# Kernel tuning notes

Hardware: AMD Instinct MI355X
Metric: run time of the kernel (lower is better)

The kernel has to match this reference:

```python
import jax, jax.numpy as jnp
import numpy as np

N_NODES = 50000
N_EDGES = 600000
K = 4
BN_EPS = 1e-5


def setup_inputs() -> dict:
    key = jax.random.key(0)
    ks = jax.random.split(key, 8)
    x = jax.random.normal(ks[0], (N_NODES, 128), dtype=jnp.float32)
    edge_index = jax.random.randint(ks[1], (2, N_EDGES), 0, N_NODES, dtype=jnp.int64)
    edge_weight = jax.random.uniform(ks[2], (N_EDGES,), dtype=jnp.float32)
    conv_w = jax.random.normal(ks[3], (10, K, 128, 128), dtype=jnp.float32)
    conv_b = jnp.zeros((10, 128), dtype=jnp.float32)
    bn_gamma = jnp.ones((10, 128), dtype=jnp.float32)
    bn_beta = jnp.zeros((10, 128), dtype=jnp.float32)
    lin_w = jax.random.normal(ks[4], (128, 16), dtype=jnp.float32)
    lin_b = jnp.zeros((16,), dtype=jnp.float32)
    return {"x": x, "edge_index": edge_index, "edge_weight": edge_weight,
            "conv_w": conv_w, "conv_b": conv_b, "bn_gamma": bn_gamma,
            "bn_beta": bn_beta, "lin_w": lin_w, "lin_b": lin_b}


def _cheb_norm(edge_index, edge_weight, n_nodes):
    # PyG ChebConv with lambda_max=2, sym normalization:
    # L_hat = 2L/lambda_max - I = -D^{-1/2} A D^{-1/2}, zero diagonal.
    row, col = edge_index[0], edge_index[1]
    w = jnp.where(row == col, 0.0, edge_weight)  # remove_self_loops
    deg = jax.ops.segment_sum(w, row, num_segments=n_nodes)
    dis = jnp.where(deg > 0, jax.lax.rsqrt(jnp.where(deg > 0, deg, 1.0)), 0.0)
    norm = -dis[row] * w * dis[col]
    return norm


def _propagate(h, norm, src, dst, n_nodes):
    # (L_hat h)[i] = sum over edges (src->dst==i) norm_e * h[src_e]
    return jax.ops.segment_sum(norm[:, None] * h[src], dst, num_segments=n_nodes)


def _cheb_conv(h, norm, src, dst, W, b, n_nodes):
    # W: [K, F_in, F_out]; Chebyshev recurrence T0=h, T1=Lh, Tk=2L T_{k-1} - T_{k-2}
    Tx0 = h
    out = Tx0 @ W[0]
    Tx1 = _propagate(Tx0, norm, src, dst, n_nodes)
    out = out + Tx1 @ W[1]
    for k in range(2, W.shape[0]):
        Tx2 = 2.0 * _propagate(Tx1, norm, src, dst, n_nodes) - Tx0
        out = out + Tx2 @ W[k]
        Tx0, Tx1 = Tx1, Tx2
    return out + b


def _batchnorm(h, gamma, beta):
    mean = jnp.mean(h, axis=0)
    var = jnp.mean(jnp.square(h - mean), axis=0)  # biased, as torch BN
    return gamma * (h - mean) * jax.lax.rsqrt(var + BN_EPS) + beta


def reference(x, edge_index, edge_weight, conv_w, conv_b, bn_gamma, bn_beta, lin_w, lin_b):
    n_nodes = x.shape[0]
    src, dst = edge_index[0], edge_index[1]
    norm = _cheb_norm(edge_index, edge_weight, n_nodes)
    h = x
    for i in range(10):
        h = jax.nn.relu(_cheb_conv(h, norm, src, dst, conv_w[i], conv_b[i], n_nodes))
        h = _batchnorm(h, bn_gamma[i], bn_beta[i])
        # dropout: identity (eval mode / deterministic reference)
    return h @ lin_w + lin_b
```

## Files before the change

kernel.cpp:

```cpp
#include <hip/hip_runtime.h>
#include <hip/hip_bf16.h>
#include <cstddef>

#define NN 50000
#define NE 600000
#define FD 128
#define NL 10
#define BN_EPS 1e-5f
#define NBG ((NN + 127) / 128)
#define SCB ((NN + 255) / 256)
#define NBK 9

typedef _Float16 f16x8 __attribute__((ext_vector_type(8)));
typedef _Float16 f16x2 __attribute__((ext_vector_type(2)));
typedef float f32x4 __attribute__((ext_vector_type(4)));

__global__ void k_detect(const unsigned int* __restrict__ gamma_raw,
                         const unsigned int* __restrict__ idx_raw,
                         int* __restrict__ flags) {
  if (threadIdx.x == 0 && blockIdx.x == 0) {
    flags[0] = (gamma_raw[0] == 0x3F803F80u) ? 1 : 0;
    int i64 = 1;
    for (int i = 1; i < 64; i += 2)
      if (idx_raw[i] != 0u) i64 = 0;
    flags[1] = i64;
  }
}

__device__ __forceinline__ float ld_f(const void* src, int i, int isbf) {
  if (isbf) {
    unsigned int u = ((const unsigned short*)src)[i];
    return __uint_as_float(u << 16);
  }
  return ((const float*)src)[i];
}

#define R_IDX 1200000
#define R_H   4400000
#define R_EW  5000000
#define R_W   5655360
#define R_P   5661312
__global__ void k_pre(const void* __restrict__ x, const void* __restrict__ eidx,
                      const void* __restrict__ ew, const void* __restrict__ convw,
                      const void* __restrict__ convb, const void* __restrict__ gamma,
                      const void* __restrict__ beta, const void* __restrict__ linw,
                      const void* __restrict__ linb,
                      int* __restrict__ idx32, unsigned int* __restrict__ hbuf,
                      float* __restrict__ ewf, unsigned short* __restrict__ wt,
                      float* __restrict__ convbf, float* __restrict__ gammaf,
                      float* __restrict__ betaf, float* __restrict__ linwf,
                      float* __restrict__ linbf,
                      const int* __restrict__ flags) {
  int gid = blockIdx.x * 256 + threadIdx.x;
  int isbf = flags[0];
  if (gid < R_IDX) {
    if (flags[1]) idx32[gid] = (int)((const long long*)eidx)[gid];
    else          idx32[gid] = ((const int*)eidx)[gid];
  } else if (gid < R_H) {
    int i = gid - R_IDX;
    f16x2 p;
    p.x = (_Float16)ld_f(x, i * 2, isbf);
    p.y = (_Float16)ld_f(x, i * 2 + 1, isbf);
    hbuf[i] = *(unsigned int*)&p;
  } else if (gid < R_EW) {
    int i = gid - R_H;
    ewf[i] = ld_f(ew, i, isbf);
  } else if (gid < R_W) {
    int tid = gid - R_EW;
    int L = tid >> 16;
    int r16 = tid & 65535;
    int s = r16 >> 12;
    int r = r16 & 4095;
    int n = r >> 5, kk = r & 31;
    int kc = s >> 2, kb = s & 3;
    int krow = kb * 32 + kk;
    int base = (L * 4) * FD * FD;
    float v;
    if (kc == 0)
      v = ld_f(convw, base + (0 * FD + krow) * FD + n, isbf)
        - ld_f(convw, base + (2 * FD + krow) * FD + n, isbf);
    else if (kc == 1)
      v = ld_f(convw, base + (1 * FD + krow) * FD + n, isbf)
        - 3.f * ld_f(convw, base + (3 * FD + krow) * FD + n, isbf);
    else if (kc == 2)
      v = 2.f * ld_f(convw, base + (2 * FD + krow) * FD + n, isbf);
    else
      v = 4.f * ld_f(convw, base + (3 * FD + krow) * FD + n, isbf);
    _Float16 h = (_Float16)v;
    wt[tid] = *(unsigned short*)&h;
  } else if (gid < R_P) {
    int i = gid - R_W;
    if (i < 1280) convbf[i] = ld_f(convb, i, isbf);
    else if (i < 2560) gammaf[i - 1280] = ld_f(gamma, i - 1280, isbf);
    else if (i < 3840) betaf[i - 2560] = ld_f(beta, i - 2560, isbf);
    else if (i < 5888) linwf[i - 3840] = ld_f(linw, i - 3840, isbf);
    else if (i < 5904) linbf[i - 5888] = ld_f(linb, i - 5888, isbf);
  }
}

__global__ void k_deg(const int* __restrict__ src, const int* __restrict__ dst,
                      const float* __restrict__ w, float* __restrict__ deg,
                      int* __restrict__ counts, int m) {
  int e = blockIdx.x * 256 + threadIdx.x;
  if (e >= m) return;
  int s = src[e], d = dst[e];
  float ww = (s == d) ? 0.f : w[e];
  atomicAdd(&deg[s], ww);
  atomicAdd(&counts[d], 1);
}

__global__ void k_dis_scan1(float* __restrict__ deg, const int* __restrict__ counts,
                            int* __restrict__ bsum, int n) {
  __shared__ int sd[256];
  int i = blockIdx.x * 256 + threadIdx.x;
  if (i < n) {
    float d = deg[i];
    deg[i] = (d > 0.f) ? rsqrtf(d) : 0.f;
  }
  sd[threadIdx.x] = (i < n) ? counts[i] : 0;
  __syncthreads();
  for (int off = 128; off; off >>= 1) {
    if (threadIdx.x < off) sd[threadIdx.x] += sd[threadIdx.x + off];
    __syncthreads();
  }
  if (threadIdx.x == 0) bsum[blockIdx.x] = sd[0];
}

__global__ void k_scan2(const int* __restrict__ bsum, int* __restrict__ boff, int nb) {
  __shared__ int sd[256];
  int t = threadIdx.x;
  int v = (t < nb) ? bsum[t] : 0;
  sd[t] = v;
  __syncthreads();
  for (int off = 1; off < 256; off <<= 1) {
    int x = sd[t];
    int add = (t >= off) ? sd[t - off] : 0;
    __syncthreads();
    sd[t] = x + add;
    __syncthreads();
  }
  if (t < nb) boff[t] = sd[t] - v;
}

__global__ void k_scan3(const int* __restrict__ counts, const int* __restrict__ boff,
                        int* __restrict__ rowptr, int* __restrict__ cursor, int n, int m) {
  __shared__ int sd[256];
  int t = threadIdx.x;
  int i = blockIdx.x * 256 + t;
  int v = (i < n) ? counts[i] : 0;
  sd[t] = v;
  __syncthreads();
  for (int off = 1; off < 256; off <<= 1) {
    int x = sd[t];
    int add = (t >= off) ? sd[t - off] : 0;
    __syncthreads();
    sd[t] = x + add;
    __syncthreads();
  }
  if (i < n) {
    int excl = boff[blockIdx.x] + sd[t] - v;
    rowptr[i] = excl;
    cursor[i] = excl;
  }
  if (i == n - 1) rowptr[n] = m;
}

__global__ void k_fill(const int* __restrict__ src, const int* __restrict__ dst,
                       const float* __restrict__ w, const float* __restrict__ dis,
                       int* __restrict__ cursor, unsigned int* __restrict__ esw, int m) {
  int e = blockIdx.x * 256 + threadIdx.x;
  if (e >= m) return;
  int s = src[e], d = dst[e];
  float ww = (s == d) ? 0.f : w[e];
  float nv = -dis[s] * ww * dis[d];
  _Float16 hv = (_Float16)nv;
  unsigned int pk = (unsigned int)s | ((unsigned int)*(unsigned short*)&hv << 16);
  int pos = atomicAdd(&cursor[d], 1);
  esw[pos] = pk;
}

__global__ void k_rowsum(const int* __restrict__ rowptr, const unsigned int* __restrict__ esw,
                         float* __restrict__ rowsum, int* __restrict__ bcount, int n) {
  __shared__ int lcnt[NBK];
  int t = threadIdx.x;
  if (t < NBK) lcnt[t] = 0;
  __syncthreads();
  int node = blockIdx.x * 256 + t;
  if (node < n) {
    int beg = rowptr[node], end = rowptr[node + 1];
    float s = 0.f;
    for (int e = beg; e < end; e++) {
      unsigned short hw = (unsigned short)(esw[e] >> 16);
      s += (float)*(_Float16*)&hw;
    }
    rowsum[node] = s;
    int b = (end - beg + 7) >> 3; if (b > 8) b = 8;
    atomicAdd(&lcnt[b], 1);
  }
  __syncthreads();
  if (t < NBK && lcnt[t]) atomicAdd(&bcount[t], lcnt[t]);
}

__global__ void k_border(const int* __restrict__ rowptr, const int* __restrict__ bcount,
                         int* __restrict__ bcur, int* __restrict__ order, int n) {
  __shared__ int lcnt[NBK], lbase[NBK], sboff[NBK];
  int t = threadIdx.x;
  if (t < NBK) lcnt[t] = 0;
  if (t == 0) {
    int run = 0;
    for (int i = 0; i < NBK; i++) { sboff[i] = run; run += bcount[i]; }
  }
  __syncthreads();
  int node = blockIdx.x * 256 + t;
  int b = 0, my = 0;
  if (node < n) {
    int cn = rowptr[node + 1] - rowptr[node];
    b = (cn + 7) >> 3; if (b > 8) b = 8;
    my = atomicAdd(&lcnt[b], 1);
  }
  __syncthreads();
  if (t < NBK) lbase[t] = lcnt[t] ? atomicAdd(&bcur[t], lcnt[t]) : 0;
  __syncthreads();
  if (node < n) order[sboff[b] + lbase[b] + my] = node;
}

template <int MODE>
__global__ __launch_bounds__(256) void k_prop(const uint4* __restrict__ h128,
                                              const int* __restrict__ order,
                                              const int* __restrict__ rowptr,
                                              const unsigned int* __restrict__ esw,
                                              const float* __restrict__ stats,
                                              const float* __restrict__ gamma,
                                              const float* __restrict__ beta,
                                              const float* __restrict__ rowsum,
                                              uint4* __restrict__ out128,
                                              float invN, int n) {
  __shared__ float ls[128], lt[128];
  int tid = threadIdx.x;
  if (MODE == 0) {
    if (tid < 128) {
      float s, t;
      if (stats) {
        float mean = stats[tid] * invN;
        float var = stats[128 + tid] * invN - mean * mean;
        s = gamma[tid] * rsqrtf(var + BN_EPS);
        t = beta[tid] - mean * s;
      } else { s = 1.f; t = 0.f; }
      ls[tid] = s; lt[tid] = t;
    }
    __syncthreads();
  }
  int idx = blockIdx.x * 16 + (tid >> 4);
  int l = tid & 15;
  if (idx >= n) return;
  int node = order[idx];
  int beg = rowptr[node], end = rowptr[node + 1];
  float a[8];
#pragma unroll
  for (int i = 0; i < 8; i++) a[i] = 0.f;
  for (int e = beg; e < end; e += 8) {
    int   s_[8];
    float w_[8];
#pragma unroll
    for (int j = 0; j < 8; j++) {
      int ee = e + j;
      int ec = (ee < end) ? ee : (end - 1);
      unsigned int m = esw[ec];
      s_[j] = m & 0xFFFFu;
      unsigned short hw = (unsigned short)(m >> 16);
      w_[j] = (ee < end) ? (float)*(_Float16*)&hw : 0.f;
    }
    uint4 g[8];
#pragma unroll
    for (int j = 0; j < 8; j++) g[j] = h128[(size_t)s_[j] * 16 + l];
#pragma unroll
    for (int j = 0; j < 8; j++) {
      f16x2 u0 = *(f16x2*)&g[j].x;
      f16x2 u1 = *(f16x2*)&g[j].y;
      f16x2 u2 = *(f16x2*)&g[j].z;
      f16x2 u3 = *(f16x2*)&g[j].w;
      a[0] = fmaf(w_[j], (float)u0.x, a[0]);
      a[1] = fmaf(w_[j], (float)u0.y, a[1]);
      a[2] = fmaf(w_[j], (float)u1.x, a[2]);
      a[3] = fmaf(w_[j], (float)u1.y, a[3]);
      a[4] = fmaf(w_[j], (float)u2.x, a[4]);
      a[5] = fmaf(w_[j], (float)u2.y, a[5]);
      a[6] = fmaf(w_[j], (float)u3.x, a[6]);
      a[7] = fmaf(w_[j], (float)u3.y, a[7]);
    }
  }
  if (MODE == 0) {
    float rs = rowsum[node];
#pragma unroll
    for (int j = 0; j < 8; j++) a[j] = ls[l * 8 + j] * a[j] + lt[l * 8 + j] * rs;
  }
  f16x2 o0, o1, o2, o3;
  o0.x = (_Float16)a[0]; o0.y = (_Float16)a[1];
  o1.x = (_Float16)a[2]; o1.y = (_Float16)a[3];
  o2.x = (_Float16)a[4]; o2.y = (_Float16)a[5];
  o3.x = (_Float16)a[6]; o3.y = (_Float16)a[7];
  uint4 o;
  o.x = *(unsigned int*)&o0; o.y = *(unsigned int*)&o1;
  o.z = *(unsigned int*)&o2; o.w = *(unsigned int*)&o3;
  out128[(size_t)node * 16 + l] = o;
}

__global__ __launch_bounds__(256) void k_gemm(const unsigned short* __restrict__ T0h,
                                              const unsigned short* __restrict__ T1h,
                                              const unsigned short* __restrict__ T2h,
                                              const unsigned short* __restrict__ T3h,
                                              const unsigned short* __restrict__ Wt,
                                              const float* __restrict__ bias,
                                              const float* __restrict__ statsPrev,
                                              const float* __restrict__ gamma,
                                              const float* __restrict__ beta,
                                              unsigned short* __restrict__ outh,
                                              float* __restrict__ stats,
                                              float invN, int n) {
  __shared__ unsigned short ldsB[2][128 * 40];
  __shared__ float lps[4][128], lqs[4][128];
  __shared__ float ls[128], lt[128];
  int tid = threadIdx.x;
  int wid = tid >> 6, lane = tid & 63;
  int ln = lane & 15, kg = lane >> 4;
  int r0 = blockIdx.x * 128 + wid * 32;

  if (tid < 128) {
    float s, t;
    if (statsPrev) {
      float mean = statsPrev[tid] * invN;
      float var = statsPrev[128 + tid] * invN - mean * mean;
      s = gamma[tid] * rsqrtf(var + BN_EPS);
      t = beta[tid] - mean * s;
    } else { s = 1.f; t = 0.f; }
    ls[tid] = s; lt[tid] = t;
  }

  f32x4 acc[2][8];
#pragma unroll
  for (int rb = 0; rb < 2; rb++)
#pragma unroll
    for (int nb = 0; nb < 8; nb++) acc[rb][nb] = (f32x4){0.f, 0.f, 0.f, 0.f};

  {
    const uint4* g = (const uint4*)(Wt);
    uint4 a = g[tid], b = g[tid + 256];
    *(uint4*)&ldsB[0][(tid >> 2) * 40 + (tid & 3) * 8] = a;
    *(uint4*)&ldsB[0][((tid >> 2) + 64) * 40 + (tid & 3) * 8] = b;
  }
  __syncthreads();

  int rowA0 = r0 + ln;       if (rowA0 >= n) rowA0 = n - 1;
  int rowA1 = r0 + 16 + ln;  if (rowA1 >= n) rowA1 = n - 1;

#pragma unroll
  for (int kc = 0; kc < 4; ++kc) {
    const unsigned short* T = (kc == 0) ? T0h : (kc == 1) ? T1h : (kc == 2) ? T2h : T3h;
#pragma unroll
    for (int kb = 0; kb < 4; ++kb) {
      const int s = kc * 4 + kb;
      const int cur = s & 1;
      uint4 st0, st1;
      if (s < 15) {
        const uint4* g = (const uint4*)(Wt + (s + 1) * 4096);
        st0 = g[tid]; st1 = g[tid + 256];
      }
      f16x8 a0 = *(const f16x8*)(T + (size_t)rowA0 * FD + kb * 32 + kg * 8);
      f16x8 a1 = *(const f16x8*)(T + (size_t)rowA1 * FD + kb * 32 + kg * 8);
      if (kc == 0) {
#pragma unroll
        for (int j = 0; j < 8; j++) {
          int f = kb * 32 + kg * 8 + j;
          a0[j] = (_Float16)(ls[f] * (float)a0[j] + lt[f]);
          a1[j] = (_Float16)(ls[f] * (float)a1[j] + lt[f]);
        }
      }
      f16x8 bf[8];
#pragma unroll
      for (int nb = 0; nb < 8; nb++)
        bf[nb] = *(const f16x8*)&ldsB[cur][(nb * 16 + ln) * 40 + kg * 8];
#pragma unroll
      for (int nb = 0; nb < 8; nb++) {
        acc[0][nb] = __builtin_amdgcn_mfma_f32_16x16x32_f16(a0, bf[nb], acc[0][nb], 0, 0, 0);
        acc[1][nb] = __builtin_amdgcn_mfma_f32_16x16x32_f16(a1, bf[nb], acc[1][nb], 0, 0, 0);
      }
      if (s < 15) {
        *(uint4*)&ldsB[cur ^ 1][(tid >> 2) * 40 + (tid & 3) * 8] = st0;
        *(uint4*)&ldsB[cur ^ 1][((tid >> 2) + 64) * 40 + (tid & 3) * 8] = st1;
      }
      __syncthreads();
    }
  }

  float psum[8], psq[8];
#pragma unroll
  for (int nb = 0; nb < 8; nb++) { psum[nb] = 0.f; psq[nb] = 0.f; }
#pragma unroll
  for (int rb = 0; rb < 2; rb++) {
#pragma unroll
    for (int nb = 0; nb < 8; nb++) {
      int col = nb * 16 + ln;
      float bs = bias[col];
#pragma unroll
      for (int r = 0; r < 4; r++) {
        int row = r0 + rb * 16 + kg * 4 + r;
        if (row < n) {
          float v = acc[rb][nb][r] + bs;
          v = fmaxf(v, 0.f);
          _Float16 hv = (_Float16)v;
          outh[(size_t)row * FD + col] = *(unsigned short*)&hv;
          psum[nb] += v;
          psq[nb] += v * v;
        }
      }
    }
  }
#pragma unroll
  for (int nb = 0; nb < 8; nb++) {
    float sv = psum[nb], qv = psq[nb];
    sv += __shfl_xor(sv, 16); sv += __shfl_xor(sv, 32);
    qv += __shfl_xor(qv, 16); qv += __shfl_xor(qv, 32);
    if (kg == 0) { lps[wid][nb * 16 + ln] = sv; lqs[wid][nb * 16 + ln] = qv; }
  }
  __syncthreads();
  if (tid < 128) {
    float sv = lps[0][tid] + lps[1][tid] + lps[2][tid] + lps[3][tid];
    atomicAdd(&stats[tid], sv);
  } else {
    int c = tid - 128;
    float qv = lqs[0][c] + lqs[1][c] + lqs[2][c] + lqs[3][c];
    atomicAdd(&stats[128 + c], qv);
  }
}

__global__ void k_final(const unsigned short* __restrict__ h, const float* __restrict__ w,
                        const float* __restrict__ b, const float* __restrict__ stats,
                        const float* __restrict__ gamma, const float* __restrict__ beta,
                        void* __restrict__ out, float invN, int n,
                        const int* __restrict__ flags) {
  __shared__ float lw[2048];
  __shared__ float ls[128], lt[128];
  for (int i = threadIdx.x; i < 2048; i += 256) lw[i] = w[i];
  if (threadIdx.x < 128) {
    int f = threadIdx.x;
    float mean = stats[f] * invN;
    float var = stats[128 + f] * invN - mean * mean;
    float s = gamma[f] * rsqrtf(var + BN_EPS);
    ls[f] = s;
    lt[f] = beta[f] - mean * s;
  }
  __syncthreads();
  int node = blockIdx.x * 256 + threadIdx.x;
  if (node >= n) return;
  float acc[16];
#pragma unroll
  for (int c = 0; c < 16; c++) acc[c] = b[c];
  const f16x8* hr = (const f16x8*)(h + (size_t)node * FD);
#pragma unroll 2
  for (int k8 = 0; k8 < 16; k8++) {
    f16x8 hv = hr[k8];
#pragma unroll
    for (int j = 0; j < 8; j++) {
      int f = k8 * 8 + j;
      float x = ls[f] * (float)hv[j] + lt[f];
#pragma unroll
      for (int c = 0; c < 16; c++) acc[c] = fmaf(x, lw[f * 16 + c], acc[c]);
    }
  }
  int isbf = flags[0];
  for (int c = 0; c < 16; c++) {
    int idx = node * 16 + c;
    if (isbf) ((__hip_bfloat16*)out)[idx] = __float2bfloat16(acc[c]);
    else      ((float*)out)[idx] = acc[c];
  }
}

extern "C" void kernel_launch(void* const* d_in, const int* in_sizes, int n_in,
                              void* d_out, int out_size, void* d_ws, size_t ws_size,
                              hipStream_t stream) {
  char* p = (char*)d_ws;
  auto take = [&](size_t bytes) -> void* {
    void* r = (void*)p;
    p += (bytes + 255) & ~size_t(255);
    return r;
  };
  int*   flags  = (int*)  take(64);
  int*   idx32  = (int*)  take(sizeof(int) * 2 * NE);
  float* ewf    = (float*)take(sizeof(float) * NE);
  unsigned short* wtws = (unsigned short*)take(sizeof(short) * NL * 16 * 4096);
  float* convbf = (float*)take(sizeof(float) * NL * FD);
  float* gammaf = (float*)take(sizeof(float) * NL * FD);
  float* betaf  = (float*)take(sizeof(float) * NL * FD);
  float* linwf  = (float*)take(sizeof(float) * FD * 16);
  float* linbf  = (float*)take(sizeof(float) * 16);
  size_t zbsz   = sizeof(float) * NN + sizeof(int) * NN + sizeof(float) * NL * 256 + 128;
  char*  zb     = (char*) take(zbsz);
  float* deg    = (float*)zb;
  int*   counts = (int*)  (zb + sizeof(float) * NN);
  float* stats  = (float*)(zb + sizeof(float) * NN + sizeof(int) * NN);
  int*   bcount = (int*)  (zb + sizeof(float) * NN + sizeof(int) * NN + sizeof(float) * NL * 256);
  int*   bcur   = bcount + 16;
  float* rowsum = (float*)take(sizeof(float) * NN);
  int*   rowptr = (int*)  take(sizeof(int) * (NN + 1));
  int*   cursor = (int*)  take(sizeof(int) * NN);
  int*   bsum   = (int*)  take(sizeof(int) * SCB);
  int*   boff   = (int*)  take(sizeof(int) * SCB);
  int*   order  = (int*)  take(sizeof(int) * NN);
  unsigned int* esw = (unsigned int*)take(sizeof(int) * NE);
  unsigned int* hbuf = (unsigned int*)take(sizeof(int) * (size_t)NN * 64);
  unsigned int* t1   = (unsigned int*)take(sizeof(int) * (size_t)NN * 64);
  unsigned int* t2   = (unsigned int*)take(sizeof(int) * (size_t)NN * 64);
  unsigned int* t3   = (unsigned int*)take(sizeof(int) * (size_t)NN * 64);

  k_detect<<<1, 64, 0, stream>>>((const unsigned int*)d_in[5], (const unsigned int*)d_in[1], flags);

  k_pre<<<(R_P + 255) / 256, 256, 0, stream>>>(d_in[0], d_in[1], d_in[2], d_in[3], d_in[4],
                                               d_in[5], d_in[6], d_in[7], d_in[8],
                                               idx32, hbuf, ewf, wtws,
                                               convbf, gammaf, betaf, linwf, linbf, flags);

  hipMemsetAsync(zb, 0, zbsz, stream);

  const int* srcI = idx32;
  const int* dstI = idx32 + NE;
  k_deg<<<(NE + 255) / 256, 256, 0, stream>>>(srcI, dstI, ewf, deg, counts, NE);
  k_dis_scan1<<<SCB, 256, 0, stream>>>(deg, counts, bsum, NN);
  k_scan2<<<1, 256, 0, stream>>>(bsum, boff, SCB);
  k_scan3<<<SCB, 256, 0, stream>>>(counts, boff, rowptr, cursor, NN, NE);
  k_fill<<<(NE + 255) / 256, 256, 0, stream>>>(srcI, dstI, ewf, deg, cursor, esw, NE);
  k_rowsum<<<SCB, 256, 0, stream>>>(rowptr, esw, rowsum, bcount, NN);
  k_border<<<SCB, 256, 0, stream>>>(rowptr, bcount, bcur, order, NN);

  const float invN = 1.0f / NN;
  for (int L = 0; L < NL; ++L) {
    const unsigned short* Wt = wtws + (size_t)L * 16 * 4096;
    const float* sPrev = (L == 0) ? nullptr : stats + (size_t)(L - 1) * 256;
    const float* gPrev = gammaf + (size_t)(L ? L - 1 : 0) * FD;
    const float* bPrev = betaf + (size_t)(L ? L - 1 : 0) * FD;
    k_prop<0><<<(NN + 15) / 16, 256, 0, stream>>>((const uint4*)hbuf, order, rowptr, esw,
                                                  sPrev, gPrev, bPrev, rowsum, (uint4*)t1, invN, NN);
    k_prop<1><<<(NN + 15) / 16, 256, 0, stream>>>((const uint4*)t1, order, rowptr, esw,
                                                  nullptr, nullptr, nullptr, nullptr, (uint4*)t2, invN, NN);
    k_prop<1><<<(NN + 15) / 16, 256, 0, stream>>>((const uint4*)t2, order, rowptr, esw,
                                                  nullptr, nullptr, nullptr, nullptr, (uint4*)t3, invN, NN);
    k_gemm<<<NBG, 256, 0, stream>>>((const unsigned short*)hbuf, (const unsigned short*)t1,
                                    (const unsigned short*)t2, (const unsigned short*)t3,
                                    Wt, convbf + L * FD, sPrev, gPrev, bPrev,
                                    (unsigned short*)hbuf, stats + (size_t)L * 256, invN, NN);
  }

  k_final<<<(NN + 255) / 256, 256, 0, stream>>>((const unsigned short*)hbuf, linwf, linbf,
                                                stats + (size_t)(NL - 1) * 256,
                                                gammaf + (size_t)(NL - 1) * FD,
                                                betaf + (size_t)(NL - 1) * FD,
                                                d_out, invN, NN, flags);
}
```

Measured before the change: 1.131 ms.

## Fuse degree computation into preprocessing and halve GEMM block size

Folds the degree/count atomics from a separate k_deg kernel into k_pre, which now reads each edge's src/dst/weight once. The zero-fill memset is moved before k_pre so the atomics accumulate into cleared buffers. Separately, the per-layer GEMM now runs 128-thread blocks covering 64 rows instead of 256-thread blocks covering 128 rows. That doubles the block count, which can improve load balance across CUs, but each block loads the full weight tile for half as many rows, raising weight-load traffic per row.

```diff
diff --git a/kernel.cpp b/kernel.cpp
--- a/kernel.cpp
+++ b/kernel.cpp
@@ -7,7 +7,7 @@
 #define FD 128
 #define NL 10
 #define BN_EPS 1e-5f
-#define NBG ((NN + 127) / 128)
+#define NBG ((NN + 63) / 64)
 #define SCB ((NN + 255) / 256)
 #define NBK 9
 
@@ -35,11 +35,10 @@
   return ((const float*)src)[i];
 }
 
-#define R_IDX 1200000
-#define R_H   4400000
-#define R_EW  5000000
-#define R_W   5655360
-#define R_P   5661312
+#define R_E   600000
+#define R_H   3800000
+#define R_W   4455360
+#define R_P   4461312
 __global__ void k_pre(const void* __restrict__ x, const void* __restrict__ eidx,
                       const void* __restrict__ ew, const void* __restrict__ convw,
                       const void* __restrict__ convb, const void* __restrict__ gamma,
@@ -50,23 +49,35 @@
                       float* __restrict__ convbf, float* __restrict__ gammaf,
                       float* __restrict__ betaf, float* __restrict__ linwf,
                       float* __restrict__ linbf,
+                      float* __restrict__ deg, int* __restrict__ counts,
                       const int* __restrict__ flags) {
   int gid = blockIdx.x * 256 + threadIdx.x;
   int isbf = flags[0];
-  if (gid < R_IDX) {
-    if (flags[1]) idx32[gid] = (int)((const long long*)eidx)[gid];
-    else          idx32[gid] = ((const int*)eidx)[gid];
+  if (gid < R_E) {
+    int e = gid;
+    int s, d;
+    if (flags[1]) {
+      s = (int)((const long long*)eidx)[e];
+      d = (int)((const long long*)eidx)[NE + e];
+    } else {
+      s = ((const int*)eidx)[e];
+      d = ((const int*)eidx)[NE + e];
+    }
+    float w = ld_f(ew, e, isbf);
+    idx32[e] = s;
+    idx32[NE + e] = d;
+    ewf[e] = w;
+    float ww = (s == d) ? 0.f : w;
+    atomicAdd(&deg[s], ww);
+    atomicAdd(&counts[d], 1);
   } else if (gid < R_H) {
-    int i = gid - R_IDX;
+    int i = gid - R_E;
     f16x2 p;
     p.x = (_Float16)ld_f(x, i * 2, isbf);
     p.y = (_Float16)ld_f(x, i * 2 + 1, isbf);
     hbuf[i] = *(unsigned int*)&p;
-  } else if (gid < R_EW) {
-    int i = gid - R_H;
-    ewf[i] = ld_f(ew, i, isbf);
   } else if (gid < R_W) {
-    int tid = gid - R_EW;
+    int tid = gid - R_H;
     int L = tid >> 16;
     int r16 = tid & 65535;
     int s = r16 >> 12;
@@ -98,17 +109,6 @@
   }
 }
 
-__global__ void k_deg(const int* __restrict__ src, const int* __restrict__ dst,
-                      const float* __restrict__ w, float* __restrict__ deg,
-                      int* __restrict__ counts, int m) {
-  int e = blockIdx.x * 256 + threadIdx.x;
-  if (e >= m) return;
-  int s = src[e], d = dst[e];
-  float ww = (s == d) ? 0.f : w[e];
-  atomicAdd(&deg[s], ww);
-  atomicAdd(&counts[d], 1);
-}
-
 __global__ void k_dis_scan1(float* __restrict__ deg, const int* __restrict__ counts,
                             int* __restrict__ bsum, int n) {
   __shared__ int sd[256];
@@ -305,7 +305,7 @@
   out128[(size_t)node * 16 + l] = o;
 }
 
-__global__ __launch_bounds__(256) void k_gemm(const unsigned short* __restrict__ T0h,
+__global__ __launch_bounds__(128) void k_gemm(const unsigned short* __restrict__ T0h,
                                               const unsigned short* __restrict__ T1h,
                                               const unsigned short* __restrict__ T2h,
                                               const unsigned short* __restrict__ T3h,
@@ -318,12 +318,12 @@
                                               float* __restrict__ stats,
                                               float invN, int n) {
   __shared__ unsigned short ldsB[2][128 * 40];
-  __shared__ float lps[4][128], lqs[4][128];
+  __shared__ float lps[2][128], lqs[2][128];
   __shared__ float ls[128], lt[128];
   int tid = threadIdx.x;
   int wid = tid >> 6, lane = tid & 63;
   int ln = lane & 15, kg = lane >> 4;
-  int r0 = blockIdx.x * 128 + wid * 32;
+  int r0 = blockIdx.x * 64 + wid * 32;
 
   if (tid < 128) {
     float s, t;
@@ -344,9 +344,11 @@
 
   {
     const uint4* g = (const uint4*)(Wt);
-    uint4 a = g[tid], b = g[tid + 256];
-    *(uint4*)&ldsB[0][(tid >> 2) * 40 + (tid & 3) * 8] = a;
-    *(uint4*)&ldsB[0][((tid >> 2) + 64) * 40 + (tid & 3) * 8] = b;
+#pragma unroll
+    for (int i = 0; i < 4; i++) {
+      uint4 a = g[tid + i * 128];
+      *(uint4*)&ldsB[0][((tid >> 2) + i * 32) * 40 + (tid & 3) * 8] = a;
+    }
   }
   __syncthreads();
 
@@ -360,10 +362,10 @@
     for (int kb = 0; kb < 4; ++kb) {
       const int s = kc * 4 + kb;
       const int cur = s & 1;
-      uint4 st0, st1;
+      uint4 st0, st1, st2, st3;
       if (s < 15) {
         const uint4* g = (const uint4*)(Wt + (s + 1) * 4096);
-        st0 = g[tid]; st1 = g[tid + 256];
+        st0 = g[tid]; st1 = g[tid + 128]; st2 = g[tid + 256]; st3 = g[tid + 384];
       }
       f16x8 a0 = *(const f16x8*)(T + (size_t)rowA0 * FD + kb * 32 + kg * 8);
       f16x8 a1 = *(const f16x8*)(T + (size_t)rowA1 * FD + kb * 32 + kg * 8);
@@ -386,7 +388,9 @@
       }
       if (s < 15) {
         *(uint4*)&ldsB[cur ^ 1][(tid >> 2) * 40 + (tid & 3) * 8] = st0;
-        *(uint4*)&ldsB[cur ^ 1][((tid >> 2) + 64) * 40 + (tid & 3) * 8] = st1;
+        *(uint4*)&ldsB[cur ^ 1][((tid >> 2) + 32) * 40 + (tid & 3) * 8] = st1;
+        *(uint4*)&ldsB[cur ^ 1][((tid >> 2) + 64) * 40 + (tid & 3) * 8] = st2;
+        *(uint4*)&ldsB[cur ^ 1][((tid >> 2) + 96) * 40 + (tid & 3) * 8] = st3;
       }
       __syncthreads();
     }
@@ -424,12 +428,8 @@
   }
   __syncthreads();
   if (tid < 128) {
-    float sv = lps[0][tid] + lps[1][tid] + lps[2][tid] + lps[3][tid];
-    atomicAdd(&stats[tid], sv);
-  } else {
-    int c = tid - 128;
-    float qv = lqs[0][c] + lqs[1][c] + lqs[2][c] + lqs[3][c];
-    atomicAdd(&stats[128 + c], qv);
+    atomicAdd(&stats[tid], lps[0][tid] + lps[1][tid]);
+    atomicAdd(&stats[128 + tid], lqs[0][tid] + lqs[1][tid]);
   }
 }
 
@@ -514,16 +514,16 @@
 
   k_detect<<<1, 64, 0, stream>>>((const unsigned int*)d_in[5], (const unsigned int*)d_in[1], flags);
 
+  hipMemsetAsync(zb, 0, zbsz, stream);
+
   k_pre<<<(R_P + 255) / 256, 256, 0, stream>>>(d_in[0], d_in[1], d_in[2], d_in[3], d_in[4],
                                                d_in[5], d_in[6], d_in[7], d_in[8],
                                                idx32, hbuf, ewf, wtws,
-                                               convbf, gammaf, betaf, linwf, linbf, flags);
-
-  hipMemsetAsync(zb, 0, zbsz, stream);
+                                               convbf, gammaf, betaf, linwf, linbf,
+                                               deg, counts, flags);
 
   const int* srcI = idx32;
   const int* dstI = idx32 + NE;
-  k_deg<<<(NE + 255) / 256, 256, 0, stream>>>(srcI, dstI, ewf, deg, counts, NE);
   k_dis_scan1<<<SCB, 256, 0, stream>>>(deg, counts, bsum, NN);
   k_scan2<<<1, 256, 0, stream>>>(bsum, boff, SCB);
   k_scan3<<<SCB, 256, 0, stream>>>(counts, boff, rowptr, cursor, NN, NE);
@@ -543,7 +543,7 @@
                                                   nullptr, nullptr, nullptr, nullptr, (uint4*)t2, invN, NN);
     k_prop<1><<<(NN + 15) / 16, 256, 0, stream>>>((const uint4*)t2, order, rowptr, esw,
                                                   nullptr, nullptr, nullptr, nullptr, (uint4*)t3, invN, NN);
-    k_gemm<<<NBG, 256, 0, stream>>>((const unsigned short*)hbuf, (const unsigned short*)t1,
+    k_gemm<<<NBG, 128, 0, stream>>>((const unsigned short*)hbuf, (const unsigned short*)t1,
                                     (const unsigned short*)t2, (const unsigned short*)t3,
                                     Wt, convbf + L * FD, sPrev, gPrev, bPrev,
                                     (unsigned short*)hbuf, stats + (size_t)L * 256, invN, NN);
```

Measured after the change: 1.223 ms. +8.1%, slower.
